# Kernel optimization log

Measured on AMD Instinct MI355X. Metric: run time of the kernel, lower is better.

## Reference

```python
import jax, jax.numpy as jnp
import numpy as np

# Workspace layout (static slice bounds, per init_kwargs)
SS, SE = 0, 512        # spoke
HPS, HPE = 512, 768    # hub private
HSS, HSE = 768, 1024   # hub shared
TS, TE = 1024, 1088    # tag
HS, HE = 512, 1024     # full hub (priv + shared) for the read path

B, T, D_STATE, D_MODEL, D_LATENT = 8, 4096, 1088, 1024, 128


def setup_inputs() -> dict:
    key = jax.random.key(0)
    ks = jax.random.split(key, 10)
    scale = 0.02  # typical init scale for learned projections
    return {
        "S": jax.random.normal(ks[0], (B, T, D_STATE), jnp.float32),
        "w_spoke": jax.random.normal(ks[1], (B, T, SE - SS), jnp.float32),
        "w_hub_priv": jax.random.normal(ks[2], (B, T, HPE - HPS), jnp.float32),
        "w_hub_shared": jax.random.normal(ks[3], (B, T, HSE - HSS), jnp.float32),
        "tag": jax.random.normal(ks[4], (B, T, TE - TS), jnp.float32),
        "W_read": jax.random.normal(ks[5], (D_MODEL, D_STATE), jnp.float32) * scale,
        "cache": jnp.zeros((B, T, D_LATENT), jnp.float32),
        "latent": jax.random.normal(ks[6], (B, T, D_LATENT), jnp.float32),
        "Wk": jax.random.normal(ks[7], (D_MODEL, D_LATENT), jnp.float32) * scale,
        "Wv": jax.random.normal(ks[8], (D_MODEL, D_LATENT), jnp.float32) * scale,
    }


def reference(S, w_spoke, w_hub_priv, w_hub_shared, tag, W_read, cache, latent, Wk, Wv):
    # --- fused_workspace_write: four independent slice-adds into S ---
    S = S.at[:, :, SS:SE].add(w_spoke)
    S = S.at[:, :, HPS:HPE].add(w_hub_priv)
    S = S.at[:, :, HSS:HSE].add(w_hub_shared)
    S = S.at[:, :, TS:TE].add(tag)

    # --- fused_workspace_read: concat(spoke, hub, tag) then F.linear(., W_read) ---
    readable = jnp.concatenate(
        [S[:, :, SS:SE], S[:, :, HS:HE], S[:, :, TS:TE]], axis=-1
    )  # (B, T, D_STATE)
    out = jnp.einsum("btr,dr->btd", readable, W_read)  # (B, T, D_MODEL)

    # --- CWTLatentCache.update: overwrite latents at start_position=0 ---
    cache = jax.lax.dynamic_update_slice(cache, latent, (0, 0, 0))

    # --- K/V reconstruction from compressed latents via up-projections ---
    k = jnp.einsum("btl,dl->btd", cache, Wk)  # (B, T, D_MODEL)
    v = jnp.einsum("btl,dl->btd", cache, Wv)  # (B, T, D_MODEL)
    return (out, k, v)
```

## Files before the change

kernel.cpp:

```cpp
#include <hip/hip_runtime.h>

typedef __attribute__((ext_vector_type(8))) _Float16 half8;
typedef __attribute__((ext_vector_type(2))) __fp16 half2r;
typedef __attribute__((ext_vector_type(4))) float f32x4;

#define AS1 __attribute__((address_space(1)))
#define AS3 __attribute__((address_space(3)))

union H2U { half2r h; unsigned int u; };
union Frag { half8 v; unsigned long long d[2]; };

__device__ __forceinline__ unsigned int pk(float a, float b) {
    H2U x; x.h = __builtin_amdgcn_cvt_pkrtz(a, b); return x.u;
}

__device__ __forceinline__ void gload_lds16(const void* g, void* l) {
    __builtin_amdgcn_global_load_lds((const AS1 unsigned int*)g,
                                     (AS3 unsigned int*)l, 16, 0, 0);
}

#define WS2_OFF 2228224
#define W2_ROWB 256

__device__ __forceinline__ void pick_w(int ks, const float* wsp, const float* whp,
                                       const float* whs, const float* wtg,
                                       const float*& wbase, int& wstr, int& wko) {
    if (ks < 8)       { wbase = wsp; wstr = 512; wko = ks * 64; }
    else if (ks < 12) { wbase = whp; wstr = 256; wko = ks * 64 - 512; }
    else if (ks < 16) { wbase = whs; wstr = 256; wko = ks * 64 - 768; }
    else              { wbase = wtg; wstr = 64;  wko = 0; }
}

__device__ __forceinline__ size_t pf_addr(int r, int kt) {
    int kh = kt >> 5, k32 = kt & 31;
    int u = (k32 & 15) >> 2, pos8 = (k32 >> 4) << 3;
    return ((size_t)r << 7) + ((size_t)((((kh << 2) | u) ^ (r & 7)) << 4)) + pos8;
}

__global__ __launch_bounds__(256) void prep_w(const float* __restrict__ Wr,
                                              const float* __restrict__ Wk,
                                              const float* __restrict__ Wv,
                                              char* __restrict__ ws) {
    int id = blockIdx.x * 256 + threadIdx.x;
    if (id < 272 * 1024) {
        int n = id / 272;
        int k = (id % 272) * 4;
        f32x4 w = *(const f32x4*)(Wr + (size_t)n * 1088 + k);
        uint2 q; q.x = pk(w.x, w.y); q.y = pk(w.z, w.w);
        int t = k >> 6;
        size_t off = ((size_t)((n >> 7) * 17 + t) << 14) + pf_addr(n & 127, k & 63);
        *(uint2*)(ws + off) = q;
    } else {
        int j = id - 272 * 1024;
        int r = j >> 5;
        int k = (j & 31) << 2;
        const float* src = (r < 1024) ? (Wk + (size_t)r * 128 + k)
                                      : (Wv + (size_t)(r - 1024) * 128 + k);
        f32x4 w = *(const f32x4*)src;
        uint2 q; q.x = pk(w.x, w.y); q.y = pk(w.z, w.w);
        size_t off = WS2_OFF + (size_t)r * W2_ROWB + ((k >> 6) << 7)
                   + (((k & 63) << 1) ^ ((r & 7) << 4));
        *(uint2*)(ws + off) = q;
    }
}

__global__ __launch_bounds__(256)
void fuse_a(const float* __restrict__ S, const float* __restrict__ wsp,
            const float* __restrict__ whp, const float* __restrict__ whs,
            const float* __restrict__ wtg, char* __restrict__ a16) {
    int u = blockIdx.x * 256 + threadIdx.x;
    int row = u / 272;
    int rem = u % 272;
    int ks = rem >> 4;
    int k4 = (rem & 15) << 2;

    const float* wbase; int wstr, wko;
    pick_w(ks, wsp, whp, whs, wtg, wbase, wstr, wko);

    f32x4 s4 = *(const f32x4*)(S + (size_t)row * 1088 + ks * 64 + k4);
    f32x4 w4 = *(const f32x4*)(wbase + (size_t)row * wstr + wko + k4);
    uint2 q; q.x = pk(s4.x + w4.x, s4.y + w4.y);
             q.y = pk(s4.z + w4.z, s4.w + w4.w);
    size_t off = ((size_t)((row >> 7) * 17 + ks) << 14) + pf_addr(row & 127, k4);
    *(uint2*)(a16 + off) = q;
}

__global__ __launch_bounds__(512, 2)
void gemm_read(const char* __restrict__ a16, const char* __restrict__ wws,
               float* __restrict__ out) {
    extern __shared__ char lds[];

    int bid = blockIdx.x;
    int wg   = (bid & 7) * 64 + (bid >> 3);
    int mblk = wg >> 2, nblk = wg & 3;
    int m0 = mblk << 8, n0 = nblk << 8;

    int tid = threadIdx.x;
    int lane = tid & 63, wid = tid >> 6;
    int wm = (wid >> 2) << 7, wn = (wid & 3) << 6;
    int lp = lane & 15, lg = lane >> 4;

    int aoff = (wid >> 2) * 16384;
    int boff = 32768 + (wn >> 7) * 16384;
    int cb64 = wn & 64;

    const char* srcH[4];
    srcH[0] = a16 + ((size_t)((m0 >> 7) * 17) << 14);
    srcH[1] = srcH[0] + (17 << 14);
    srcH[2] = wws + ((size_t)((n0 >> 7) * 17) << 14);
    srcH[3] = srcH[2] + (17 << 14);

    f32x4 acc[8][4] = {};
    Frag af[4], bf[4];

#define STAGE(T, H, DB) do {                                               \
        const char* s_ = srcH[H] + ((size_t)(T) << 14);                    \
        char* d_ = lds + (DB) + (H) * 16384;                               \
        gload_lds16(s_ + tid * 16, d_ + tid * 16);                         \
        gload_lds16(s_ + 8192 + tid * 16, d_ + 8192 + tid * 16);           \
    } while (0)

#define LOADA(MH, KH, BB) do {                                             \
        _Pragma("unroll")                                                  \
        for (int f = 0; f < 4; ++f) {                                      \
            int r_ = (MH) * 64 + f * 16 + lp;                              \
            af[f] = *(const Frag*)(lds + (BB) + aoff + (r_ << 7)           \
                     + ((((((KH) << 2) | lg) ^ (r_ & 7))) << 4));          \
        }                                                                  \
    } while (0)

#define LOADB(KH, BB) do {                                                 \
        _Pragma("unroll")                                                  \
        for (int g = 0; g < 4; ++g) {                                      \
            int c_ = cb64 + g * 16 + lp;                                   \
            bf[g] = *(const Frag*)(lds + (BB) + boff + (c_ << 7)           \
                     + ((((((KH) << 2) | lg) ^ (c_ & 7))) << 4));          \
        }                                                                  \
    } while (0)

#define MFMA16(MH) do {                                                    \
        __builtin_amdgcn_s_setprio(1);                                     \
        _Pragma("unroll")                                                  \
        for (int f = 0; f < 4; ++f)                                        \
            _Pragma("unroll")                                              \
            for (int g = 0; g < 4; ++g)                                    \
                acc[(MH) * 4 + f][g] = __builtin_amdgcn_mfma_f32_16x16x32_f16( \
                    af[f].v, bf[g].v, acc[(MH) * 4 + f][g], 0, 0, 0);      \
        __builtin_amdgcn_s_setprio(0);                                     \
    } while (0)

    STAGE(0, 0, 0); STAGE(0, 1, 0); STAGE(0, 2, 0); STAGE(0, 3, 0);

    for (int t = 0; t < 16; ++t) {
        int BB = (t & 1) << 16;
        int NB = BB ^ 65536;
        STAGE(t + 1, 0, NB);
        asm volatile("s_waitcnt vmcnt(2)" ::: "memory");
        __builtin_amdgcn_s_barrier();
        LOADB(0, BB); LOADA(0, 0, BB);
        MFMA16(0);
        __builtin_amdgcn_s_barrier();
        LOADA(1, 0, BB);
        STAGE(t + 1, 1, NB);
        __builtin_amdgcn_s_barrier();
        MFMA16(1);
        __builtin_amdgcn_s_barrier();
        LOADB(1, BB); LOADA(0, 1, BB);
        STAGE(t + 1, 2, NB);
        __builtin_amdgcn_s_barrier();
        MFMA16(0);
        __builtin_amdgcn_s_barrier();
        LOADA(1, 1, BB);
        STAGE(t + 1, 3, NB);
        __builtin_amdgcn_s_barrier();
        MFMA16(1);
        __builtin_amdgcn_s_barrier();
    }
    {
        const int BB = 0;
        asm volatile("s_waitcnt vmcnt(0)" ::: "memory");
        __builtin_amdgcn_s_barrier();
        LOADB(0, BB); LOADA(0, 0, BB); MFMA16(0);
        __builtin_amdgcn_s_barrier();
        LOADA(1, 0, BB); MFMA16(1);
        __builtin_amdgcn_s_barrier();
        LOADB(1, BB); LOADA(0, 1, BB); MFMA16(0);
        __builtin_amdgcn_s_barrier();
        LOADA(1, 1, BB); MFMA16(1);
    }

    #pragma unroll
    for (int i = 0; i < 8; ++i)
        #pragma unroll
        for (int j = 0; j < 4; ++j) {
            int row = m0 + wm + i * 16 + (lg << 2);
            int col = n0 + wn + j * 16 + lp;
            float* p = out + (size_t)row * 1024 + col;
            #pragma unroll
            for (int r = 0; r < 4; ++r) p[(size_t)r * 1024] = acc[i][j][r];
        }
#undef STAGE
#undef LOADA
#undef LOADB
#undef MFMA16
}

__global__ __launch_bounds__(256, 2)
void gemm_kv(const float* __restrict__ lat, const char* __restrict__ ws2,
             float* __restrict__ outk, float* __restrict__ outv) {
    __shared__ char lds[32768];
    char* Al = lds;
    char* Bl = lds + 16384;

    int bid = blockIdx.x;
    int wg   = (bid & 7) * 512 + (bid >> 3);
    int mblk = wg >> 4, nb = wg & 15;
    int m0 = mblk << 7;
    int nrow0 = nb << 7;
    float* out = (nb < 8) ? outk : outv;
    int n0 = (nb & 7) << 7;

    int tid = threadIdx.x;
    int lane = tid & 63, wid = tid >> 6;
    int wm = (wid >> 1) << 6, wn = (wid & 1) << 6;
    int lp = lane & 15, lg = lane >> 4;

    f32x4 acc[4][4] = {};

    for (int ks = 0; ks < 2; ++ks) {
        __syncthreads();
        {
            const char* wrow = ws2 + (size_t)nrow0 * W2_ROWB + ks * 128;
            #pragma unroll
            for (int c = 0; c < 4; ++c) {
                int s = c * 4096 + wid * 1024 + lane * 16;
                int n = s >> 7, cb = s & 127;
                gload_lds16(wrow + (size_t)n * W2_ROWB + cb,
                            Bl + c * 4096 + wid * 1024);
            }
        }
        #pragma unroll
        for (int i = 0; i < 8; ++i) {
            int u = i * 256 + tid;
            int row = u >> 4;
            int k4 = (u & 15) << 2;
            f32x4 s4 = *(const f32x4*)(lat + (size_t)(m0 + row) * 128 + ks * 64 + k4);
            uint2 q; q.x = pk(s4.x, s4.y); q.y = pk(s4.z, s4.w);
            *(uint2*)(Al + (row << 7) + ((k4 << 1) ^ ((row & 7) << 4))) = q;
        }
        __syncthreads();

        #pragma unroll
        for (int b = 0; b < 2; ++b) {
            Frag af[4], bf[4];
            #pragma unroll
            for (int f = 0; f < 4; ++f) {
                int ra = wm + f * 16 + lp;  int xa = (ra & 7) << 4;
                af[f].d[0] = *(const unsigned long long*)(Al + (ra << 7) + ((b * 64 + lg * 8) ^ xa));
                af[f].d[1] = *(const unsigned long long*)(Al + (ra << 7) + ((b * 64 + 32 + lg * 8) ^ xa));
                int rb = wn + f * 16 + lp;  int xb = (rb & 7) << 4;
                bf[f].d[0] = *(const unsigned long long*)(Bl + (rb << 7) + ((b * 64 + lg * 8) ^ xb));
                bf[f].d[1] = *(const unsigned long long*)(Bl + (rb << 7) + ((b * 64 + 32 + lg * 8) ^ xb));
            }
            #pragma unroll
            for (int i = 0; i < 4; ++i)
                #pragma unroll
                for (int j = 0; j < 4; ++j)
                    acc[i][j] = __builtin_amdgcn_mfma_f32_16x16x32_f16(af[i].v, bf[j].v, acc[i][j], 0, 0, 0);
        }
    }

    #pragma unroll
    for (int i = 0; i < 4; ++i)
        #pragma unroll
        for (int j = 0; j < 4; ++j) {
            int row = m0 + wm + i * 16 + (lg << 2);
            int col = n0 + wn + j * 16 + lp;
            float* p = out + (size_t)row * 1024 + col;
            #pragma unroll
            for (int r = 0; r < 4; ++r) p[(size_t)r * 1024] = acc[i][j][r];
        }
}

extern "C" void kernel_launch(void* const* d_in, const int* in_sizes, int n_in,
                              void* d_out, int out_size, void* d_ws, size_t ws_size,
                              hipStream_t stream) {
    const float* S   = (const float*)d_in[0];
    const float* wsp = (const float*)d_in[1];
    const float* whp = (const float*)d_in[2];
    const float* whs = (const float*)d_in[3];
    const float* wtg = (const float*)d_in[4];
    const float* Wr  = (const float*)d_in[5];
    const float* lat = (const float*)d_in[7];
    const float* Wk  = (const float*)d_in[8];
    const float* Wv  = (const float*)d_in[9];
    float* out = (float*)d_out;
    char*  ws  = (char*)d_ws;

    static bool lds_init = false;
    if (!lds_init) {
        hipFuncSetAttribute(reinterpret_cast<const void*>(gemm_read),
                            hipFuncAttributeMaxDynamicSharedMemorySize, 131072);
        lds_init = true;
    }

    char* a16 = (char*)(out + 67108864ull);

    hipLaunchKernelGGL(prep_w, dim3(1344), dim3(256), 0, stream, Wr, Wk, Wv, ws);
    hipLaunchKernelGGL(fuse_a, dim3(34816), dim3(256), 0, stream,
                       S, wsp, whp, whs, wtg, a16);
    hipLaunchKernelGGL(gemm_read, dim3(512), dim3(512), 131072, stream,
                       a16, ws, out);
    hipLaunchKernelGGL(gemm_kv, dim3(4096), dim3(256), 0, stream,
                       lat, ws + WS2_OFF, out + 33554432ull, out + 67108864ull);
}
```

Before: 253.1 us.

## Fuse A-operand prep with K/V GEMM in one interleaved launch

Merges the elementwise add-and-convert kernel with the K/V up-projection GEMM into one grid, interleaving 17 prep blocks with K/V GEMM blocks per group. The memory-bound conversion then overlaps with MFMA-heavy GEMM work, and one launch is removed. When the workspace is large enough, the fp16 A buffer moves out of the V output region so both K and V can be computed in the fused launch. Otherwise only K is fused and V runs after the read GEMM. Risks: the per-block branch gives heterogeneous block shapes, and the fuse blocks now reserve 32KB of LDS, which may reduce their occupancy.

```diff
diff --git a/kernel.cpp b/kernel.cpp
--- a/kernel.cpp
+++ b/kernel.cpp
@@ -20,7 +20,9 @@
 }
 
 #define WS2_OFF 2228224
+#define WS2_SZ  524288
 #define W2_ROWB 256
+#define A16_SZ  71303168ull
 
 __device__ __forceinline__ void pick_w(int ks, const float* wsp, const float* whp,
                                        const float* whs, const float* wtg,
@@ -64,11 +66,10 @@
     }
 }
 
-__global__ __launch_bounds__(256)
-void fuse_a(const float* __restrict__ S, const float* __restrict__ wsp,
-            const float* __restrict__ whp, const float* __restrict__ whs,
-            const float* __restrict__ wtg, char* __restrict__ a16) {
-    int u = blockIdx.x * 256 + threadIdx.x;
+__device__ __forceinline__
+void fuse_body(int u, const float* __restrict__ S, const float* __restrict__ wsp,
+               const float* __restrict__ whp, const float* __restrict__ whs,
+               const float* __restrict__ wtg, char* __restrict__ a16) {
     int row = u / 272;
     int rem = u % 272;
     int ks = rem >> 4;
@@ -83,6 +84,110 @@
              q.y = pk(s4.z + w4.z, s4.w + w4.w);
     size_t off = ((size_t)((row >> 7) * 17 + ks) << 14) + pf_addr(row & 127, k4);
     *(uint2*)(a16 + off) = q;
+}
+
+__device__ __forceinline__
+void kv_body(int mblk, int nb, const float* __restrict__ lat,
+             const char* __restrict__ ws2, float* __restrict__ outk,
+             float* __restrict__ outv, char* lds) {
+    char* Al = lds;
+    char* Bl = lds + 16384;
+
+    int m0 = mblk << 7;
+    int nrow0 = nb << 7;
+    float* out = (nb < 8) ? outk : outv;
+    int n0 = (nb & 7) << 7;
+
+    int tid = threadIdx.x;
+    int lane = tid & 63, wid = tid >> 6;
+    int wm = (wid >> 1) << 6, wn = (wid & 1) << 6;
+    int lp = lane & 15, lg = lane >> 4;
+
+    f32x4 acc[4][4] = {};
+
+    for (int ks = 0; ks < 2; ++ks) {
+        __syncthreads();
+        {
+            const char* wrow = ws2 + (size_t)nrow0 * W2_ROWB + ks * 128;
+            #pragma unroll
+            for (int c = 0; c < 4; ++c) {
+                int s = c * 4096 + wid * 1024 + lane * 16;
+                int n = s >> 7, cb = s & 127;
+                gload_lds16(wrow + (size_t)n * W2_ROWB + cb,
+                            Bl + c * 4096 + wid * 1024);
+            }
+        }
+        #pragma unroll
+        for (int i = 0; i < 8; ++i) {
+            int u = i * 256 + tid;
+            int row = u >> 4;
+            int k4 = (u & 15) << 2;
+            f32x4 s4 = *(const f32x4*)(lat + (size_t)(m0 + row) * 128 + ks * 64 + k4);
+            uint2 q; q.x = pk(s4.x, s4.y); q.y = pk(s4.z, s4.w);
+            *(uint2*)(Al + (row << 7) + ((k4 << 1) ^ ((row & 7) << 4))) = q;
+        }
+        __syncthreads();
+
+        #pragma unroll
+        for (int b = 0; b < 2; ++b) {
+            Frag af[4], bf[4];
+            #pragma unroll
+            for (int f = 0; f < 4; ++f) {
+                int ra = wm + f * 16 + lp;  int xa = (ra & 7) << 4;
+                af[f].d[0] = *(const unsigned long long*)(Al + (ra << 7) + ((b * 64 + lg * 8) ^ xa));
+                af[f].d[1] = *(const unsigned long long*)(Al + (ra << 7) + ((b * 64 + 32 + lg * 8) ^ xa));
+                int rb = wn + f * 16 + lp;  int xb = (rb & 7) << 4;
+                bf[f].d[0] = *(const unsigned long long*)(Bl + (rb << 7) + ((b * 64 + lg * 8) ^ xb));
+                bf[f].d[1] = *(const unsigned long long*)(Bl + (rb << 7) + ((b * 64 + 32 + lg * 8) ^ xb));
+            }
+            #pragma unroll
+            for (int i = 0; i < 4; ++i)
+                #pragma unroll
+                for (int j = 0; j < 4; ++j)
+                    acc[i][j] = __builtin_amdgcn_mfma_f32_16x16x32_f16(af[i].v, bf[j].v, acc[i][j], 0, 0, 0);
+        }
+    }
+
+    #pragma unroll
+    for (int i = 0; i < 4; ++i)
+        #pragma unroll
+        for (int j = 0; j < 4; ++j) {
+            int row = m0 + wm + i * 16 + (lg << 2);
+            int col = n0 + wn + j * 16 + lp;
+            float* p = out + (size_t)row * 1024 + col;
+            #pragma unroll
+            for (int r = 0; r < 4; ++r) p[(size_t)r * 1024] = acc[i][j][r];
+        }
+}
+
+__global__ __launch_bounds__(256, 2)
+void fuse_kv(const float* __restrict__ S, const float* __restrict__ wsp,
+             const float* __restrict__ whp, const float* __restrict__ whs,
+             const float* __restrict__ wtg, char* __restrict__ a16,
+             const float* __restrict__ lat, const char* __restrict__ ws2,
+             float* __restrict__ outk, float* __restrict__ outv,
+             int kvpg, int gsz) {
+    __shared__ char lds[32768];
+    int bid = blockIdx.x;
+    int g = bid / gsz, slot = bid - g * gsz;
+    if (slot < 17) {
+        fuse_body((g * 17 + slot) * 256 + threadIdx.x, S, wsp, whp, whs, wtg, a16);
+    } else {
+        int idx = g * kvpg + (slot - 17);
+        int mblk, nb;
+        if (kvpg == 2) { int wg = (idx & 7) * 512 + (idx >> 3); mblk = wg >> 4; nb = wg & 15; }
+        else           { int wg = (idx & 7) * 256 + (idx >> 3); mblk = wg >> 3; nb = wg & 7; }
+        kv_body(mblk, nb, lat, ws2, outk, outv, lds);
+    }
+}
+
+__global__ __launch_bounds__(256, 2)
+void gemm_v(const float* __restrict__ lat, const char* __restrict__ ws2,
+            float* __restrict__ outk, float* __restrict__ outv) {
+    __shared__ char lds[32768];
+    int idx = blockIdx.x;
+    int wg = (idx & 7) * 256 + (idx >> 3);
+    kv_body(wg >> 3, 8 + (wg & 7), lat, ws2, outk, outv, lds);
 }
 
 __global__ __launch_bounds__(512, 2)
@@ -203,83 +308,6 @@
 #undef LOADA
 #undef LOADB
 #undef MFMA16
-}
-
-__global__ __launch_bounds__(256, 2)
-void gemm_kv(const float* __restrict__ lat, const char* __restrict__ ws2,
-             float* __restrict__ outk, float* __restrict__ outv) {
-    __shared__ char lds[32768];
-    char* Al = lds;
-    char* Bl = lds + 16384;
-
-    int bid = blockIdx.x;
-    int wg   = (bid & 7) * 512 + (bid >> 3);
-    int mblk = wg >> 4, nb = wg & 15;
-    int m0 = mblk << 7;
-    int nrow0 = nb << 7;
-    float* out = (nb < 8) ? outk : outv;
-    int n0 = (nb & 7) << 7;
-
-    int tid = threadIdx.x;
-    int lane = tid & 63, wid = tid >> 6;
-    int wm = (wid >> 1) << 6, wn = (wid & 1) << 6;
-    int lp = lane & 15, lg = lane >> 4;
-
-    f32x4 acc[4][4] = {};
-
-    for (int ks = 0; ks < 2; ++ks) {
-        __syncthreads();
-        {
-            const char* wrow = ws2 + (size_t)nrow0 * W2_ROWB + ks * 128;
-            #pragma unroll
-            for (int c = 0; c < 4; ++c) {
-                int s = c * 4096 + wid * 1024 + lane * 16;
-                int n = s >> 7, cb = s & 127;
-                gload_lds16(wrow + (size_t)n * W2_ROWB + cb,
-                            Bl + c * 4096 + wid * 1024);
-            }
-        }
-        #pragma unroll
-        for (int i = 0; i < 8; ++i) {
-            int u = i * 256 + tid;
-            int row = u >> 4;
-            int k4 = (u & 15) << 2;
-            f32x4 s4 = *(const f32x4*)(lat + (size_t)(m0 + row) * 128 + ks * 64 + k4);
-            uint2 q; q.x = pk(s4.x, s4.y); q.y = pk(s4.z, s4.w);
-            *(uint2*)(Al + (row << 7) + ((k4 << 1) ^ ((row & 7) << 4))) = q;
-        }
-        __syncthreads();
-
-        #pragma unroll
-        for (int b = 0; b < 2; ++b) {
-            Frag af[4], bf[4];
-            #pragma unroll
-            for (int f = 0; f < 4; ++f) {
-                int ra = wm + f * 16 + lp;  int xa = (ra & 7) << 4;
-                af[f].d[0] = *(const unsigned long long*)(Al + (ra << 7) + ((b * 64 + lg * 8) ^ xa));
-                af[f].d[1] = *(const unsigned long long*)(Al + (ra << 7) + ((b * 64 + 32 + lg * 8) ^ xa));
-                int rb = wn + f * 16 + lp;  int xb = (rb & 7) << 4;
-                bf[f].d[0] = *(const unsigned long long*)(Bl + (rb << 7) + ((b * 64 + lg * 8) ^ xb));
-                bf[f].d[1] = *(const unsigned long long*)(Bl + (rb << 7) + ((b * 64 + 32 + lg * 8) ^ xb));
-            }
-            #pragma unroll
-            for (int i = 0; i < 4; ++i)
-                #pragma unroll
-                for (int j = 0; j < 4; ++j)
-                    acc[i][j] = __builtin_amdgcn_mfma_f32_16x16x32_f16(af[i].v, bf[j].v, acc[i][j], 0, 0, 0);
-        }
-    }
-
-    #pragma unroll
-    for (int i = 0; i < 4; ++i)
-        #pragma unroll
-        for (int j = 0; j < 4; ++j) {
-            int row = m0 + wm + i * 16 + (lg << 2);
-            int col = n0 + wn + j * 16 + lp;
-            float* p = out + (size_t)row * 1024 + col;
-            #pragma unroll
-            for (int r = 0; r < 4; ++r) p[(size_t)r * 1024] = acc[i][j][r];
-        }
 }
 
 extern "C" void kernel_launch(void* const* d_in, const int* in_sizes, int n_in,
@@ -297,6 +325,9 @@
     float* out = (float*)d_out;
     char*  ws  = (char*)d_ws;
 
+    float* outk = out + 33554432ull;
+    float* outv = out + 67108864ull;
+
     static bool lds_init = false;
     if (!lds_init) {
         hipFuncSetAttribute(reinterpret_cast<const void*>(gemm_read),
@@ -304,13 +335,26 @@
         lds_init = true;
     }
 
-    char* a16 = (char*)(out + 67108864ull);
+    const size_t A16_WS_OFF = (size_t)WS2_OFF + WS2_SZ;
+    const size_t ws_need = A16_WS_OFF + A16_SZ;
 
     hipLaunchKernelGGL(prep_w, dim3(1344), dim3(256), 0, stream, Wr, Wk, Wv, ws);
-    hipLaunchKernelGGL(fuse_a, dim3(34816), dim3(256), 0, stream,
-                       S, wsp, whp, whs, wtg, a16);
-    hipLaunchKernelGGL(gemm_read, dim3(512), dim3(512), 131072, stream,
-                       a16, ws, out);
-    hipLaunchKernelGGL(gemm_kv, dim3(4096), dim3(256), 0, stream,
-                       lat, ws + WS2_OFF, out + 33554432ull, out + 67108864ull);
-}
+
+    if (ws_size >= ws_need) {
+        char* a16 = ws + A16_WS_OFF;
+        hipLaunchKernelGGL(fuse_kv, dim3(2048 * 19), dim3(256), 0, stream,
+                           S, wsp, whp, whs, wtg, a16,
+                           lat, ws + WS2_OFF, outk, outv, 2, 19);
+        hipLaunchKernelGGL(gemm_read, dim3(512), dim3(512), 131072, stream,
+                           a16, ws, out);
+    } else {
+        char* a16 = (char*)outv;
+        hipLaunchKernelGGL(fuse_kv, dim3(2048 * 18), dim3(256), 0, stream,
+                           S, wsp, whp, whs, wtg, a16,
+                           lat, ws + WS2_OFF, outk, outv, 1, 18);
+        hipLaunchKernelGGL(gemm_read, dim3(512), dim3(512), 131072, stream,
+                           a16, ws, out);
+        hipLaunchKernelGGL(gemm_v, dim3(2048), dim3(256), 0, stream,
+                           lat, ws + WS2_OFF, outk, outv);
+    }
+}
```

Result: faster. 229.3 us (median of 2 runs) (-9.4%).

## Fuse workspace add and fp16 conversion into read GEMM A-tile loading

Applied to the files above, without the earlier changes.

Removes the separate fuse_a pass that wrote an fp16 packed copy of S+writes to global memory. The GEMM now loads S and the write slices in fp32 straight into registers, adds and converts them, then stores them into LDS in the swizzled layout, while B keeps using direct global-to-LDS loads. The inner loop is also restructured into one barrier pair per k-step instead of many interleaved barriers. This avoids an extra write and read of the A matrix, but each output tile now re-reads fp32 A across the four N blocks and needs more registers.

```diff
diff --git a/kernel.cpp b/kernel.cpp
--- a/kernel.cpp
+++ b/kernel.cpp
@@ -31,10 +31,10 @@
     else              { wbase = wtg; wstr = 64;  wko = 0; }
 }
 
-__device__ __forceinline__ size_t pf_addr(int r, int kt) {
+__device__ __forceinline__ int pf_addr(int r, int kt) {
     int kh = kt >> 5, k32 = kt & 31;
     int u = (k32 & 15) >> 2, pos8 = (k32 >> 4) << 3;
-    return ((size_t)r << 7) + ((size_t)((((kh << 2) | u) ^ (r & 7)) << 4)) + pos8;
+    return (r << 7) + (((((kh << 2) | u) ^ (r & 7))) << 4) + pos8;
 }
 
 __global__ __launch_bounds__(256) void prep_w(const float* __restrict__ Wr,
@@ -64,30 +64,11 @@
     }
 }
 
-__global__ __launch_bounds__(256)
-void fuse_a(const float* __restrict__ S, const float* __restrict__ wsp,
-            const float* __restrict__ whp, const float* __restrict__ whs,
-            const float* __restrict__ wtg, char* __restrict__ a16) {
-    int u = blockIdx.x * 256 + threadIdx.x;
-    int row = u / 272;
-    int rem = u % 272;
-    int ks = rem >> 4;
-    int k4 = (rem & 15) << 2;
-
-    const float* wbase; int wstr, wko;
-    pick_w(ks, wsp, whp, whs, wtg, wbase, wstr, wko);
-
-    f32x4 s4 = *(const f32x4*)(S + (size_t)row * 1088 + ks * 64 + k4);
-    f32x4 w4 = *(const f32x4*)(wbase + (size_t)row * wstr + wko + k4);
-    uint2 q; q.x = pk(s4.x + w4.x, s4.y + w4.y);
-             q.y = pk(s4.z + w4.z, s4.w + w4.w);
-    size_t off = ((size_t)((row >> 7) * 17 + ks) << 14) + pf_addr(row & 127, k4);
-    *(uint2*)(a16 + off) = q;
-}
-
 __global__ __launch_bounds__(512, 2)
-void gemm_read(const char* __restrict__ a16, const char* __restrict__ wws,
-               float* __restrict__ out) {
+void gemm_read_f(const float* __restrict__ S, const float* __restrict__ wsp,
+                 const float* __restrict__ whp, const float* __restrict__ whs,
+                 const float* __restrict__ wtg, const char* __restrict__ wws,
+                 float* __restrict__ out) {
     extern __shared__ char lds[];
 
     int bid = blockIdx.x;
@@ -104,20 +85,46 @@
     int boff = 32768 + (wn >> 7) * 16384;
     int cb64 = wn & 64;
 
-    const char* srcH[4];
-    srcH[0] = a16 + ((size_t)((m0 >> 7) * 17) << 14);
-    srcH[1] = srcH[0] + (17 << 14);
-    srcH[2] = wws + ((size_t)((n0 >> 7) * 17) << 14);
-    srcH[3] = srcH[2] + (17 << 14);
-
+    const char* srcB0 = wws + ((size_t)((n0 >> 7) * 17) << 14);
+    const char* srcB1 = srcB0 + (17 << 14);
+
+    int rbase = tid >> 4;
+    int k4 = (tid & 15) << 2;
+
+    f32x4 sreg[8], wreg[8];
     f32x4 acc[8][4] = {};
     Frag af[4], bf[4];
 
-#define STAGE(T, H, DB) do {                                               \
-        const char* s_ = srcH[H] + ((size_t)(T) << 14);                    \
-        char* d_ = lds + (DB) + (H) * 16384;                               \
-        gload_lds16(s_ + tid * 16, d_ + tid * 16);                         \
-        gload_lds16(s_ + 8192 + tid * 16, d_ + 8192 + tid * 16);           \
+#define ALOAD(T) do {                                                      \
+        const float* wbase; int wstr, wko;                                 \
+        pick_w((T), wsp, whp, whs, wtg, wbase, wstr, wko);                 \
+        _Pragma("unroll")                                                  \
+        for (int c = 0; c < 8; ++c) {                                      \
+            int row = m0 + rbase + c * 32;                                 \
+            sreg[c] = *(const f32x4*)(S + (size_t)row * 1088 + (T) * 64 + k4); \
+            wreg[c] = *(const f32x4*)(wbase + (size_t)row * wstr + wko + k4);  \
+        }                                                                  \
+    } while (0)
+
+#define AWRITE(DB) do {                                                    \
+        _Pragma("unroll")                                                  \
+        for (int c = 0; c < 8; ++c) {                                      \
+            int row = rbase + c * 32;                                      \
+            uint2 q;                                                       \
+            q.x = pk(sreg[c].x + wreg[c].x, sreg[c].y + wreg[c].y);        \
+            q.y = pk(sreg[c].z + wreg[c].z, sreg[c].w + wreg[c].w);        \
+            *(uint2*)(lds + (DB) + ((row >> 7) << 14)                      \
+                      + pf_addr(row & 127, k4)) = q;                       \
+        }                                                                  \
+    } while (0)
+
+#define BSTAGE(T, DB) do {                                                 \
+        const char* s0_ = srcB0 + ((size_t)(T) << 14);                     \
+        const char* s1_ = srcB1 + ((size_t)(T) << 14);                     \
+        gload_lds16(s0_ + tid * 16,        lds + (DB) + 32768 + tid * 16); \
+        gload_lds16(s0_ + 8192 + tid * 16, lds + (DB) + 40960 + tid * 16); \
+        gload_lds16(s1_ + tid * 16,        lds + (DB) + 49152 + tid * 16); \
+        gload_lds16(s1_ + 8192 + tid * 16, lds + (DB) + 57344 + tid * 16); \
     } while (0)
 
 #define LOADA(MH, KH, BB) do {                                             \
@@ -149,44 +156,35 @@
         __builtin_amdgcn_s_setprio(0);                                     \
     } while (0)
 
-    STAGE(0, 0, 0); STAGE(0, 1, 0); STAGE(0, 2, 0); STAGE(0, 3, 0);
-
-    for (int t = 0; t < 16; ++t) {
+    ALOAD(0);
+    BSTAGE(0, 0);
+    AWRITE(0);
+    asm volatile("s_waitcnt lgkmcnt(0)" ::: "memory");
+    __builtin_amdgcn_s_barrier();
+
+    for (int t = 0; t < 17; ++t) {
         int BB = (t & 1) << 16;
         int NB = BB ^ 65536;
-        STAGE(t + 1, 0, NB);
-        asm volatile("s_waitcnt vmcnt(2)" ::: "memory");
+        if (t < 16) {
+            ALOAD(t + 1);
+            BSTAGE(t + 1, NB);
+            asm volatile("s_waitcnt vmcnt(20)" ::: "memory");
+        } else {
+            asm volatile("s_waitcnt vmcnt(0)" ::: "memory");
+        }
         __builtin_amdgcn_s_barrier();
-        LOADB(0, BB); LOADA(0, 0, BB);
-        MFMA16(0);
+
+        LOADB(0, BB); LOADA(0, 0, BB); MFMA16(0);
+        LOADA(1, 0, BB);               MFMA16(1);
+        LOADB(1, BB); LOADA(0, 1, BB); MFMA16(0);
+        LOADA(1, 1, BB);               MFMA16(1);
+
+        if (t < 16) {
+            asm volatile("s_waitcnt vmcnt(4)" ::: "memory");
+            AWRITE(NB);
+            asm volatile("s_waitcnt lgkmcnt(0)" ::: "memory");
+        }
         __builtin_amdgcn_s_barrier();
-        LOADA(1, 0, BB);
-        STAGE(t + 1, 1, NB);
-        __builtin_amdgcn_s_barrier();
-        MFMA16(1);
-        __builtin_amdgcn_s_barrier();
-        LOADB(1, BB); LOADA(0, 1, BB);
-        STAGE(t + 1, 2, NB);
-        __builtin_amdgcn_s_barrier();
-        MFMA16(0);
-        __builtin_amdgcn_s_barrier();
-        LOADA(1, 1, BB);
-        STAGE(t + 1, 3, NB);
-        __builtin_amdgcn_s_barrier();
-        MFMA16(1);
-        __builtin_amdgcn_s_barrier();
-    }
-    {
-        const int BB = 0;
-        asm volatile("s_waitcnt vmcnt(0)" ::: "memory");
-        __builtin_amdgcn_s_barrier();
-        LOADB(0, BB); LOADA(0, 0, BB); MFMA16(0);
-        __builtin_amdgcn_s_barrier();
-        LOADA(1, 0, BB); MFMA16(1);
-        __builtin_amdgcn_s_barrier();
-        LOADB(1, BB); LOADA(0, 1, BB); MFMA16(0);
-        __builtin_amdgcn_s_barrier();
-        LOADA(1, 1, BB); MFMA16(1);
     }
 
     #pragma unroll
@@ -199,7 +197,9 @@
             #pragma unroll
             for (int r = 0; r < 4; ++r) p[(size_t)r * 1024] = acc[i][j][r];
         }
-#undef STAGE
+#undef ALOAD
+#undef AWRITE
+#undef BSTAGE
 #undef LOADA
 #undef LOADB
 #undef MFMA16
@@ -297,20 +297,19 @@
     float* out = (float*)d_out;
     char*  ws  = (char*)d_ws;
 
+    float* outk = out + 33554432ull;
+    float* outv = out + 67108864ull;
+
     static bool lds_init = false;
     if (!lds_init) {
-        hipFuncSetAttribute(reinterpret_cast<const void*>(gemm_read),
+        hipFuncSetAttribute(reinterpret_cast<const void*>(gemm_read_f),
                             hipFuncAttributeMaxDynamicSharedMemorySize, 131072);
         lds_init = true;
     }
 
-    char* a16 = (char*)(out + 67108864ull);
-
     hipLaunchKernelGGL(prep_w, dim3(1344), dim3(256), 0, stream, Wr, Wk, Wv, ws);
-    hipLaunchKernelGGL(fuse_a, dim3(34816), dim3(256), 0, stream,
-                       S, wsp, whp, whs, wtg, a16);
-    hipLaunchKernelGGL(gemm_read, dim3(512), dim3(512), 131072, stream,
-                       a16, ws, out);
+    hipLaunchKernelGGL(gemm_read_f, dim3(512), dim3(512), 131072, stream,
+                       S, wsp, whp, whs, wtg, ws, out);
     hipLaunchKernelGGL(gemm_kv, dim3(4096), dim3(256), 0, stream,
-                       lat, ws + WS2_OFF, out + 33554432ull, out + 67108864ull);
-}
+                       lat, ws + WS2_OFF, outk, outv);
+}
```

Result: slower. 358.1 us (+41.5%).
